# Kernel tuning notes

Measured on AMD Instinct MI355X. Metric: run time of the kernel, lower is better.

## Reference

```python
import jax, jax.numpy as jnp
import numpy as np

BATCH, T, N_INP, N_HID = 32, 512, 128, 1024
DT = 0.042
RHO = 0.99
INPUT_SCALING = 1.0
THRESHOLD = 0.5
RESET = 0.0
R_ = 1.0   # resistance
C_ = 1.0   # capacity
P = 0.5
HARMONIC = N_HID * P          # scalar, as in source: n_hid * p
SPIKING = N_HID - HARMONIC    # scalar, as in source


def setup_inputs() -> dict:
    key = jax.random.key(0)
    k1, k2, k3, k4, k5 = jax.random.split(key, 5)
    x = jax.random.normal(k1, (BATCH, T, N_INP), dtype=jnp.float32)
    # input-to-hidden in (0, input_scaling), per torch.rand * input_scaling
    x2h = jax.random.uniform(k2, (N_INP, N_HID), dtype=jnp.float32) * INPUT_SCALING
    # hidden-to-hidden: full topology, rescaled to spectral radius rho
    W = np.asarray(jax.random.uniform(k3, (N_HID, N_HID), minval=-1.0, maxval=1.0))
    sr = float(np.max(np.abs(np.linalg.eigvals(W))))
    h2h = jnp.asarray(W * (RHO / sr), dtype=jnp.float32)
    # gamma/epsilon sampled per-unit from uniform ranges (tuple branch of __init__)
    gamma = jax.random.uniform(k4, (N_HID,), minval=0.5, maxval=1.5, dtype=jnp.float32)
    epsilon = jax.random.uniform(k5, (N_HID,), minval=0.001, maxval=0.01, dtype=jnp.float32)
    bias = jnp.zeros((N_HID,), dtype=jnp.float32)
    return {"x": x, "x2h": x2h, "h2h": h2h, "gamma": gamma, "epsilon": epsilon, "bias": bias}


def reference(x, x2h, h2h, gamma, epsilon, bias):
    B = x.shape[0]
    dtype = x.dtype
    u_decay = 1.0 - R_ * C_ * DT  # u = u + R*C*dt*(-u)

    def step(carry, xt):
        hy, hz, u = carry
        # spiking_osc: threshold, reset, leak
        spike = (u > THRESHOLD).astype(dtype)
        u = jnp.where(spike == 1.0, RESET, u)
        u = u * u_decay
        # coupled-oscillator update
        drive = jnp.tanh(xt @ x2h + hy @ h2h + bias)
        hz = hz + DT * (drive - gamma * hy - (epsilon * (hz * HARMONIC) + u * SPIKING))
        hy = hy + DT * hz
        return (hy, hz, u), (hy, hz, u, spike)

    zeros = jnp.zeros((B, N_HID), dtype=dtype)
    (_, _, _), (hy_t, hz_t, u_t, spk_t) = jax.lax.scan(
        step, (zeros, zeros, zeros), jnp.swapaxes(x, 0, 1)
    )
    # (T, B, H) -> (B, T, H), matching the per-step lists of the original
    tr = lambda a: jnp.swapaxes(a, 0, 1)
    return tr(hy_t), tr(hz_t), tr(u_t), tr(spk_t)
```

## Files before the change

### kernel.cpp

```cpp
#include <hip/hip_runtime.h>
#include <cmath>

constexpr int  Bn  = 32, Tn = 512, NIn = 128, Hn = 1024;
constexpr long long TH  = (long long)Tn * Hn;
constexpr long long BTH = (long long)Bn * TH;
constexpr float DTc  = 0.042f;
constexpr float UDEC = 1.0f - 1.0f * 1.0f * DTc;
constexpr float HARM = 512.0f;
constexpr float SPIK = 512.0f;

__device__ unsigned g_tag[8 * 32 * 16];

__global__ void init_tag() {
    int i = threadIdx.x;
    __hip_atomic_store(&g_tag[i * 16], 0u,
                       __ATOMIC_RELAXED, __HIP_MEMORY_SCOPE_AGENT);
}

__global__ __launch_bounds__(256) void pre_gemm(const float* __restrict__ x,
                                                const float* __restrict__ x2h,
                                                const float* __restrict__ bias,
                                                float* __restrict__ pre) {
    __shared__ float xs[64 * 128];
    __shared__ float ws[128 * 64];
    const int tid = threadIdx.x;
    const int rb  = blockIdx.y * 64;
    const int cb  = blockIdx.x * 64;

#pragma unroll
    for (int i = 0; i < 8; ++i) {
        int idx = i * 1024 + tid * 4;
        int r = idx >> 7, k = idx & 127;
        *(float4*)(&xs[r * 128 + k]) =
            *(const float4*)(&x[(long long)(rb + r) * NIn + k]);
    }
#pragma unroll
    for (int i = 0; i < 8; ++i) {
        int idx = i * 1024 + tid * 4;
        int k = idx >> 6, c = idx & 63;
        *(float4*)(&ws[k * 64 + c]) =
            *(const float4*)(&x2h[(long long)k * Hn + cb + c]);
    }
    __syncthreads();

    const int tx = tid & 15, ty = tid >> 4;
    const int r0 = ty * 4, c0 = tx * 4;
    float acc[4][4] = {};
#pragma unroll 4
    for (int k = 0; k < 128; ++k) {
        float4 bv = *(const float4*)(&ws[k * 64 + c0]);
        float a0 = xs[(r0 + 0) * 128 + k];
        float a1 = xs[(r0 + 1) * 128 + k];
        float a2 = xs[(r0 + 2) * 128 + k];
        float a3 = xs[(r0 + 3) * 128 + k];
        acc[0][0] += a0 * bv.x; acc[0][1] += a0 * bv.y; acc[0][2] += a0 * bv.z; acc[0][3] += a0 * bv.w;
        acc[1][0] += a1 * bv.x; acc[1][1] += a1 * bv.y; acc[1][2] += a1 * bv.z; acc[1][3] += a1 * bv.w;
        acc[2][0] += a2 * bv.x; acc[2][1] += a2 * bv.y; acc[2][2] += a2 * bv.z; acc[2][3] += a2 * bv.w;
        acc[3][0] += a3 * bv.x; acc[3][1] += a3 * bv.y; acc[3][2] += a3 * bv.z; acc[3][3] += a3 * bv.w;
    }
    float4 bb = *(const float4*)(&bias[cb + c0]);
#pragma unroll
    for (int i = 0; i < 4; ++i) {
        float4 o;
        o.x = acc[i][0] + bb.x; o.y = acc[i][1] + bb.y;
        o.z = acc[i][2] + bb.z; o.w = acc[i][3] + bb.w;
        *(float4*)(&pre[(long long)(rb + r0 + i) * Hn + cb + c0]) = o;
    }
}

__global__ __launch_bounds__(256, 1) void ron_loop(const float* __restrict__ h2h,
                                                   const float* __restrict__ gam,
                                                   const float* __restrict__ eps,
                                                   float* __restrict__ out) {
    extern __shared__ float sm[];
    float* hyl  = sm;
    float* wt   = sm + 4 * 1028;
    float* part = wt;

    const int tid = threadIdx.x;
    const int bx  = blockIdx.x;
    const int bg  = bx & 7;
    const int hg  = bx >> 3;
    const int c0  = hg * 32;
    const int b0  = bg * 4;
    unsigned* mytag   = &g_tag[(bg * 32 + hg) * 16];
    unsigned* tagbase = &g_tag[bg * 32 * 16];

    float* hy_o = out;
    float* hz_o = out + BTH;
    float* u_o  = out + 2 * BTH;
    float* sp_o = out + 3 * BTH;

    for (int idx = tid; idx < 32 * 1024; idx += 256) {
        int cc2 = idx & 31, k = idx >> 5;
        wt[cc2 * 1028 + k] = h2h[(long long)k * Hn + c0 + cc2];
    }
    __syncthreads();

    const int ks   = tid & 31;
    const int tile = tid >> 5;

    float4 W[4][8];
#pragma unroll
    for (int j = 0; j < 4; ++j)
#pragma unroll
        for (int m = 0; m < 8; ++m)
            W[j][m] = *(const float4*)(wt + (tile * 4 + j) * 1028 + (ks + 32 * m) * 4);

    const float* hp0 = hyl + 0 * 1028 + ks * 4;
    const float* hp1 = hp0 + 1028;
    const float* hp2 = hp0 + 2 * 1028;
    const float* hp3 = hp0 + 3 * 1028;
    float* pw = part + (tile * 4) * 33 + ks;

    const int r  = tid & 127;
    const int cc = r & 31;
    const int bb = r >> 5;
    const int b  = b0 + bb;
    const int h  = c0 + cc;
    const float g = gam[h];
    const float e = eps[h];
    float hy = 0.0f, hz = 0.0f, u = 0.0f;

#define D4(dst, hv, wv)                                         \
    dst = fmaf(hv.x, wv.x, dst); dst = fmaf(hv.y, wv.y, dst);   \
    dst = fmaf(hv.z, wv.z, dst); dst = fmaf(hv.w, wv.w, dst)

    for (int t = 0; t < Tn; ++t) {
        float pre_v = 0.0f;
        if (tid < 128)
            pre_v = u_o[(long long)b * TH + (long long)t * Hn + h];

        float acc = 0.0f;
        if (t > 0) {
            const long long base = (long long)b0 * TH + (long long)(t - 1) * Hn + tid;
            float v[16];
#pragma unroll
            for (int i = 0; i < 16; ++i) {
                v[i] = __hip_atomic_load(
                    &hy_o[base + (long long)(i >> 2) * TH + (i & 3) * 256],
                    __ATOMIC_RELAXED, __HIP_MEMORY_SCOPE_AGENT);
            }
#pragma unroll
            for (int i = 0; i < 16; ++i)
                hyl[(i >> 2) * 1028 + (i & 3) * 256 + tid] = v[i];
            __syncthreads();

            float a00 = 0.f, a01 = 0.f, a02 = 0.f, a03 = 0.f;
            float a10 = 0.f, a11 = 0.f, a12 = 0.f, a13 = 0.f;
            float a20 = 0.f, a21 = 0.f, a22 = 0.f, a23 = 0.f;
            float a30 = 0.f, a31 = 0.f, a32 = 0.f, a33 = 0.f;
#pragma unroll
            for (int m = 0; m < 8; ++m) {
                const int o4 = m * 128;
                float4 h0 = *(const float4*)(hp0 + o4);
                float4 h1 = *(const float4*)(hp1 + o4);
                float4 h2 = *(const float4*)(hp2 + o4);
                float4 h3 = *(const float4*)(hp3 + o4);
                D4(a00, h0, W[0][m]); D4(a01, h0, W[1][m]); D4(a02, h0, W[2][m]); D4(a03, h0, W[3][m]);
                D4(a10, h1, W[0][m]); D4(a11, h1, W[1][m]); D4(a12, h1, W[2][m]); D4(a13, h1, W[3][m]);
                D4(a20, h2, W[0][m]); D4(a21, h2, W[1][m]); D4(a22, h2, W[2][m]); D4(a23, h2, W[3][m]);
                D4(a30, h3, W[0][m]); D4(a31, h3, W[1][m]); D4(a32, h3, W[2][m]); D4(a33, h3, W[3][m]);
            }

            pw[(0 * 32 + 0) * 33] = a00; pw[(0 * 32 + 1) * 33] = a01;
            pw[(0 * 32 + 2) * 33] = a02; pw[(0 * 32 + 3) * 33] = a03;
            pw[(1 * 32 + 0) * 33] = a10; pw[(1 * 32 + 1) * 33] = a11;
            pw[(1 * 32 + 2) * 33] = a12; pw[(1 * 32 + 3) * 33] = a13;
            pw[(2 * 32 + 0) * 33] = a20; pw[(2 * 32 + 1) * 33] = a21;
            pw[(2 * 32 + 2) * 33] = a22; pw[(2 * 32 + 3) * 33] = a23;
            pw[(3 * 32 + 0) * 33] = a30; pw[(3 * 32 + 1) * 33] = a31;
            pw[(3 * 32 + 2) * 33] = a32; pw[(3 * 32 + 3) * 33] = a33;
            __syncthreads();

            if (tid < 128) {
                const float* pr = part + r * 33;
                float s0 = 0.f, s1 = 0.f, s2 = 0.f, s3 = 0.f;
#pragma unroll
                for (int k = 0; k < 32; k += 4) {
                    s0 += pr[k + 0]; s1 += pr[k + 1];
                    s2 += pr[k + 2]; s3 += pr[k + 3];
                }
                acc = (s0 + s1) + (s2 + s3);
            }
        }

        float spike = 0.0f;
        long long o = 0;
        if (tid < 128) {
            spike = (u > 0.5f) ? 1.0f : 0.0f;
            u = (spike == 1.0f) ? 0.0f : u;
            u = u * UDEC;
            float drive = tanhf(acc + pre_v);
            hz = hz + DTc * (drive - g * hy - (e * (hz * HARM) + u * SPIK));
            hy = hy + DTc * hz;
            o = (long long)b * TH + (long long)t * Hn + h;
            __hip_atomic_store(&hy_o[o], hy,
                               __ATOMIC_RELAXED, __HIP_MEMORY_SCOPE_AGENT);
        }

        if (t < Tn - 1) {
            __syncthreads();
            if (tid == 0)
                __hip_atomic_store(mytag, (unsigned)(t + 1),
                                   __ATOMIC_RELAXED, __HIP_MEMORY_SCOPE_AGENT);
        }

        if (tid < 128) {
            hz_o[o] = hz;
            u_o[o]  = u;
            sp_o[o] = spike;
        }

        if (t < Tn - 1) {
            if (tid < 64) {
                const unsigned target = (unsigned)(t + 1);
                const int idx = tid & 31;
                for (;;) {
                    unsigned v = __hip_atomic_load(&tagbase[idx * 16],
                                                   __ATOMIC_RELAXED,
                                                   __HIP_MEMORY_SCOPE_AGENT);
                    if (__ballot(v < target) == 0ull) break;
                    __builtin_amdgcn_s_sleep(1);
                }
            }
            __syncthreads();
        }
    }
#undef D4
}

extern "C" void kernel_launch(void* const* d_in, const int* in_sizes, int n_in,
                              void* d_out, int out_size, void* d_ws, size_t ws_size,
                              hipStream_t stream) {
    const float* x    = (const float*)d_in[0];
    const float* x2h  = (const float*)d_in[1];
    const float* h2h  = (const float*)d_in[2];
    const float* gam  = (const float*)d_in[3];
    const float* eps  = (const float*)d_in[4];
    const float* bias = (const float*)d_in[5];
    float* out = (float*)d_out;
    float* pre = out + 2 * BTH;

    init_tag<<<1, 256, 0, stream>>>();
    pre_gemm<<<dim3(16, 256), dim3(256), 0, stream>>>(x, x2h, bias, pre);

    const unsigned smem = (4 * 1028 + 32 * 1028) * sizeof(float);
    (void)hipFuncSetAttribute((const void*)ron_loop,
                              hipFuncAttributeMaxDynamicSharedMemorySize,
                              (int)smem);
    void* args[] = {(void*)&h2h, (void*)&gam, (void*)&eps, (void*)&out};
    (void)hipLaunchCooperativeKernel((void*)ron_loop, dim3(256), dim3(256),
                                     args, smem, stream);
}
```

Measured before the change: 1.837 ms.

## Split recurrent loop across 512 blocks with two batch rows each

Adds a variant of the persistent recurrent kernel in which each block handles 2 batch rows instead of 4. The grid doubles to 512 cooperative blocks at two per CU, which halves the per-block matvec work and shared memory per step. The tag array grows to hold 16 batch groups, and the weight tile is staged in chunks so the smaller shared buffer is enough. It falls back to the old 4-row kernel if the occupancy query shows two blocks cannot fit per CU. The cost is that every block now loads the full 32-column weight slice, and more blocks take part in each group's per-step flag barrier.

```diff
diff --git a/kernel.cpp b/kernel.cpp
--- a/kernel.cpp
+++ b/kernel.cpp
@@ -9,7 +9,7 @@
 constexpr float HARM = 512.0f;
 constexpr float SPIK = 512.0f;
 
-__device__ unsigned g_tag[8 * 32 * 16];
+__device__ unsigned g_tag[16 * 32 * 16];
 
 __global__ void init_tag() {
     int i = threadIdx.x;
@@ -68,10 +68,168 @@
     }
 }
 
-__global__ __launch_bounds__(256, 1) void ron_loop(const float* __restrict__ h2h,
-                                                   const float* __restrict__ gam,
-                                                   const float* __restrict__ eps,
-                                                   float* __restrict__ out) {
+__global__ __launch_bounds__(256, 2) void ron_loop2(const float* __restrict__ h2h,
+                                                    const float* __restrict__ gam,
+                                                    const float* __restrict__ eps,
+                                                    float* __restrict__ out) {
+    extern __shared__ float sm[];
+    float* hyl  = sm;
+    float* wtb  = sm + 2 * 1028;
+    float* part = wtb;
+
+    const int tid = threadIdx.x;
+    const int bx  = blockIdx.x;
+    const int bg  = ((bx & 7) << 1) | (bx >> 8);
+    const int hg  = (bx >> 3) & 31;
+    const int c0  = hg * 32;
+    const int b0  = bg * 2;
+    unsigned* mytag   = &g_tag[(bg * 32 + hg) * 16];
+    unsigned* tagbase = &g_tag[bg * 32 * 16];
+
+    float* hy_o = out;
+    float* hz_o = out + BTH;
+    float* u_o  = out + 2 * BTH;
+    float* sp_o = out + 3 * BTH;
+
+    const int ks   = tid & 31;
+    const int tile = tid >> 5;
+
+    float4 W[4][8];
+#pragma unroll
+    for (int ch = 0; ch < 4; ++ch) {
+        for (int idx = tid; idx < 8 * 1024; idx += 256) {
+            int cc2 = idx & 7, k = idx >> 3;
+            wtb[cc2 * 1028 + k] = h2h[(long long)k * Hn + c0 + ch * 8 + cc2];
+        }
+        __syncthreads();
+        if ((tile >> 1) == ch) {
+#pragma unroll
+            for (int j = 0; j < 4; ++j)
+#pragma unroll
+                for (int m = 0; m < 8; ++m)
+                    W[j][m] = *(const float4*)(wtb + ((tile & 1) * 4 + j) * 1028
+                                               + (ks + 32 * m) * 4);
+        }
+        __syncthreads();
+    }
+
+    const float* hp0 = hyl + ks * 4;
+    const float* hp1 = hp0 + 1028;
+    float* pw = part + (tile * 4) * 33 + ks;
+
+    const int r  = tid & 63;
+    const int cc = r & 31;
+    const int bb = r >> 5;
+    const int b  = b0 + bb;
+    const int h  = c0 + cc;
+    const float g = gam[h];
+    const float e = eps[h];
+    float hy = 0.0f, hz = 0.0f, u = 0.0f;
+
+#define D4(dst, hv, wv)                                         \
+    dst = fmaf(hv.x, wv.x, dst); dst = fmaf(hv.y, wv.y, dst);   \
+    dst = fmaf(hv.z, wv.z, dst); dst = fmaf(hv.w, wv.w, dst)
+
+    for (int t = 0; t < Tn; ++t) {
+        float pre_v = 0.0f;
+        if (tid < 64)
+            pre_v = u_o[(long long)b * TH + (long long)t * Hn + h];
+
+        float acc = 0.0f;
+        if (t > 0) {
+            const long long base = (long long)b0 * TH + (long long)(t - 1) * Hn + tid;
+            float v[8];
+#pragma unroll
+            for (int i = 0; i < 8; ++i) {
+                v[i] = __hip_atomic_load(
+                    &hy_o[base + (long long)(i >> 2) * TH + (i & 3) * 256],
+                    __ATOMIC_RELAXED, __HIP_MEMORY_SCOPE_AGENT);
+            }
+#pragma unroll
+            for (int i = 0; i < 8; ++i)
+                hyl[(i >> 2) * 1028 + (i & 3) * 256 + tid] = v[i];
+            __syncthreads();
+
+            float a00 = 0.f, a01 = 0.f, a02 = 0.f, a03 = 0.f;
+            float a10 = 0.f, a11 = 0.f, a12 = 0.f, a13 = 0.f;
+#pragma unroll
+            for (int m = 0; m < 8; ++m) {
+                const int o4 = m * 128;
+                float4 h0 = *(const float4*)(hp0 + o4);
+                float4 h1 = *(const float4*)(hp1 + o4);
+                D4(a00, h0, W[0][m]); D4(a01, h0, W[1][m]);
+                D4(a02, h0, W[2][m]); D4(a03, h0, W[3][m]);
+                D4(a10, h1, W[0][m]); D4(a11, h1, W[1][m]);
+                D4(a12, h1, W[2][m]); D4(a13, h1, W[3][m]);
+            }
+
+            pw[(0 * 32 + 0) * 33] = a00; pw[(0 * 32 + 1) * 33] = a01;
+            pw[(0 * 32 + 2) * 33] = a02; pw[(0 * 32 + 3) * 33] = a03;
+            pw[(1 * 32 + 0) * 33] = a10; pw[(1 * 32 + 1) * 33] = a11;
+            pw[(1 * 32 + 2) * 33] = a12; pw[(1 * 32 + 3) * 33] = a13;
+            __syncthreads();
+
+            if (tid < 64) {
+                const float* pr = part + r * 33;
+                float s0 = 0.f, s1 = 0.f, s2 = 0.f, s3 = 0.f;
+#pragma unroll
+                for (int k = 0; k < 32; k += 4) {
+                    s0 += pr[k + 0]; s1 += pr[k + 1];
+                    s2 += pr[k + 2]; s3 += pr[k + 3];
+                }
+                acc = (s0 + s1) + (s2 + s3);
+            }
+        }
+
+        float spike = 0.0f;
+        long long o = 0;
+        if (tid < 64) {
+            spike = (u > 0.5f) ? 1.0f : 0.0f;
+            u = (spike == 1.0f) ? 0.0f : u;
+            u = u * UDEC;
+            float drive = tanhf(acc + pre_v);
+            hz = hz + DTc * (drive - g * hy - (e * (hz * HARM) + u * SPIK));
+            hy = hy + DTc * hz;
+            o = (long long)b * TH + (long long)t * Hn + h;
+            __hip_atomic_store(&hy_o[o], hy,
+                               __ATOMIC_RELAXED, __HIP_MEMORY_SCOPE_AGENT);
+        }
+
+        if (t < Tn - 1) {
+            __syncthreads();
+            if (tid == 0)
+                __hip_atomic_store(mytag, (unsigned)(t + 1),
+                                   __ATOMIC_RELAXED, __HIP_MEMORY_SCOPE_AGENT);
+        }
+
+        if (tid < 64) {
+            hz_o[o] = hz;
+            u_o[o]  = u;
+            sp_o[o] = spike;
+        }
+
+        if (t < Tn - 1) {
+            if (tid < 64) {
+                const unsigned target = (unsigned)(t + 1);
+                const int idx = tid & 31;
+                for (;;) {
+                    unsigned v = __hip_atomic_load(&tagbase[idx * 16],
+                                                   __ATOMIC_RELAXED,
+                                                   __HIP_MEMORY_SCOPE_AGENT);
+                    if (__ballot(v < target) == 0ull) break;
+                    __builtin_amdgcn_s_sleep(1);
+                }
+            }
+            __syncthreads();
+        }
+    }
+#undef D4
+}
+
+__global__ __launch_bounds__(256, 1) void ron_loop4(const float* __restrict__ h2h,
+                                                    const float* __restrict__ gam,
+                                                    const float* __restrict__ eps,
+                                                    float* __restrict__ out) {
     extern __shared__ float sm[];
     float* hyl  = sm;
     float* wt   = sm + 4 * 1028;
@@ -107,7 +265,7 @@
         for (int m = 0; m < 8; ++m)
             W[j][m] = *(const float4*)(wt + (tile * 4 + j) * 1028 + (ks + 32 * m) * 4);
 
-    const float* hp0 = hyl + 0 * 1028 + ks * 4;
+    const float* hp0 = hyl + ks * 4;
     const float* hp1 = hp0 + 1028;
     const float* hp2 = hp0 + 2 * 1028;
     const float* hp3 = hp0 + 3 * 1028;
@@ -242,14 +400,32 @@
     float* out = (float*)d_out;
     float* pre = out + 2 * BTH;
 
-    init_tag<<<1, 256, 0, stream>>>();
+    init_tag<<<1, 512, 0, stream>>>();
     pre_gemm<<<dim3(16, 256), dim3(256), 0, stream>>>(x, x2h, bias, pre);
 
-    const unsigned smem = (4 * 1028 + 32 * 1028) * sizeof(float);
-    (void)hipFuncSetAttribute((const void*)ron_loop,
+    const unsigned smem2 = (2 * 1028 + 8 * 1028) * sizeof(float);
+    const unsigned smem4 = (4 * 1028 + 32 * 1028) * sizeof(float);
+    (void)hipFuncSetAttribute((const void*)ron_loop2,
                               hipFuncAttributeMaxDynamicSharedMemorySize,
-                              (int)smem);
+                              (int)smem2);
+    (void)hipFuncSetAttribute((const void*)ron_loop4,
+                              hipFuncAttributeMaxDynamicSharedMemorySize,
+                              (int)smem4);
+
     void* args[] = {(void*)&h2h, (void*)&gam, (void*)&eps, (void*)&out};
-    (void)hipLaunchCooperativeKernel((void*)ron_loop, dim3(256), dim3(256),
-                                     args, smem, stream);
+
+    int maxb = 0;
+    hipError_t qe = hipOccupancyMaxActiveBlocksPerMultiprocessor(
+        &maxb, (const void*)ron_loop2, 256, (size_t)smem2);
+
+    bool launched = false;
+    if (qe == hipSuccess && maxb >= 2) {
+        launched = (hipLaunchCooperativeKernel((void*)ron_loop2, dim3(512),
+                                               dim3(256), args, smem2,
+                                               stream) == hipSuccess);
+    }
+    if (!launched) {
+        (void)hipLaunchCooperativeKernel((void*)ron_loop4, dim3(256),
+                                         dim3(256), args, smem4, stream);
+    }
 }
```

Measured after the change: 1.953 ms. +6.3%, slower.
